# Kernel tuning notes

Measured on AMD Instinct MI355X. Metric: run time of the kernel, lower is better.

Reference implementation:

```python
import jax, jax.numpy as jnp
import numpy as np

NQ = 8
DIM = 2 ** NQ  # 256 amplitudes
HALF_PI = float(np.pi / 2)

CNOT_M = jnp.array([[1, 0, 0, 0], [0, 1, 0, 0], [0, 0, 0, 1], [0, 0, 1, 0]], dtype=jnp.complex64)
SWAP_M = jnp.array([[1, 0, 0, 0], [0, 0, 1, 0], [0, 1, 0, 0], [0, 0, 0, 1]], dtype=jnp.complex64)

# PauliZ sign vectors per wire; wire 0 is the most-significant bit (PennyLane convention)
_bits = (np.arange(DIM)[None, :] >> (NQ - 1 - np.arange(NQ))[:, None]) & 1
ZSIGNS = jnp.asarray(1.0 - 2.0 * _bits, dtype=jnp.float32)  # [NQ, DIM]


def _rx(t):
    c = jnp.cos(0.5 * t).astype(jnp.complex64)
    s = (-1j * jnp.sin(0.5 * t)).astype(jnp.complex64)
    return jnp.stack([jnp.stack([c, s]), jnp.stack([s, c])])


def _ry(t):
    c = jnp.cos(0.5 * t).astype(jnp.complex64)
    s = jnp.sin(0.5 * t).astype(jnp.complex64)
    return jnp.stack([jnp.stack([c, -s]), jnp.stack([s, c])])


def _rz(t):
    e0 = jnp.exp(-0.5j * t).astype(jnp.complex64)
    e1 = jnp.exp(0.5j * t).astype(jnp.complex64)
    z = jnp.zeros((), jnp.complex64)
    return jnp.stack([jnp.stack([e0, z]), jnp.stack([z, e1])])


def _ixx(t):
    c = jnp.cos(0.5 * t).astype(jnp.complex64)
    s = (-1j * jnp.sin(0.5 * t)).astype(jnp.complex64)
    z = jnp.zeros((), jnp.complex64)
    return jnp.stack([jnp.stack([c, z, z, s]), jnp.stack([z, c, s, z]),
                      jnp.stack([z, s, c, z]), jnp.stack([s, z, z, c])])


def _apply_1q(psi, U, w):
    # psi: [B] + [2]*NQ ; apply 2x2 U on wire w
    psi = jnp.moveaxis(psi, 1 + w, -1)
    psi = psi @ U.T
    return jnp.moveaxis(psi, -1, 1 + w)


def _apply_2q(psi, U, w1, w2):
    # apply 4x4 U on wires (w1, w2); w1 is the more-significant wire of U
    psi = jnp.moveaxis(psi, (1 + w1, 1 + w2), (-2, -1))
    shp = psi.shape
    psi = (psi.reshape(shp[:-2] + (4,)) @ U.T).reshape(shp)
    return jnp.moveaxis(psi, (-2, -1), (1 + w1, 1 + w2))


def _edges_from_coupling(coupling):
    # Mirrors the torch code: threshold min-max normalized coupling at 0.5.
    # This is a non-differentiable, data-dependent circuit-structure decision,
    # so it is resolved on concrete values (as the Python ifs do in torch).
    c = np.asarray(jax.device_get(coupling), dtype=np.float64)
    cn = (c - c.min()) / (c.max() - c.min())
    adj = cn > 0.5
    return [(i, j) for i in range(NQ) for j in range(i + 1, NQ) if adj[i, j]]


def _conv(psi, i, j, p):
    psi = _apply_1q(psi, _rz(jnp.float32(-HALF_PI)), j)
    psi = _apply_2q(psi, CNOT_M, j, i)  # CNOT control=j target=i
    psi = _apply_1q(psi, _rz(p[0]), i)
    psi = _apply_1q(psi, _ry(p[1]), j)
    psi = _apply_2q(psi, CNOT_M, i, j)
    psi = _apply_1q(psi, _ry(p[2]), j)
    psi = _apply_2q(psi, CNOT_M, j, i)
    psi = _apply_1q(psi, _rz(jnp.float32(HALF_PI)), i)
    return psi


def _pool(psi, i, j, p):
    psi = _apply_1q(psi, _rz(jnp.float32(-HALF_PI)), j)
    psi = _apply_2q(psi, CNOT_M, j, i)
    psi = _apply_1q(psi, _rz(p[0]), i)
    psi = _apply_1q(psi, _ry(p[1]), j)
    psi = _apply_2q(psi, CNOT_M, i, j)
    psi = _apply_1q(psi, _ry(p[2]), j)
    return psi


def _circuit(x, weights, coupling, edges):
    B = x.shape[0]
    # AmplitudeEmbedding(normalize=True)
    psi = (x / jnp.linalg.norm(x, axis=1, keepdims=True)).astype(jnp.complex64)
    psi = psi.reshape((B,) + (2,) * NQ)
    for i in range(NQ):
        psi = _apply_1q(psi, _rx(weights[i]), i)
        psi = _apply_1q(psi, _ry(weights[i + NQ]), i)
        psi = _apply_1q(psi, _rz(weights[i + 2 * NQ]), i)
    for i in range(NQ):
        for j in range(i + 1, NQ):
            psi = _apply_2q(psi, _ixx(coupling[i, j]), i, j)
    widx = 3 * NQ
    for (i, j) in edges:
        nonadjacent = abs(i - j) != 1
        if nonadjacent:
            psi = _apply_2q(psi, SWAP_M, i, j)
        psi = _conv(psi, i, j, weights[widx:widx + 3])
        psi = _pool(psi, i, j, weights[widx + 3:widx + 6])
        widx += 6
        if nonadjacent:
            psi = _apply_2q(psi, SWAP_M, i, j)
    psi_f = psi.reshape(B, DIM)
    probs = psi_f.real ** 2 + psi_f.imag ** 2  # [B, DIM]
    return probs @ ZSIGNS.T  # [B, NQ] expval(PauliZ(i))


def setup_inputs() -> dict:
    B = 65536
    key = jax.random.key(0)
    k1, k2, k3 = jax.random.split(key, 3)
    x = jax.random.normal(k1, (B, DIM), dtype=jnp.float32)
    weights = jax.random.normal(k2, (3 * NQ + 6 * 28,), dtype=jnp.float32)  # 192: max edges = C(8,2)=28
    coupling = jax.random.normal(k3, (NQ, NQ), dtype=jnp.float32)
    return {"x": x, "weights": weights, "coupling": coupling}


def reference(x, weights, coupling):
    edges = _edges_from_coupling(coupling)
    return _circuit(x, weights, coupling, edges)
```

## Files before the change

kernel.cpp:

```cpp
#include <hip/hip_runtime.h>

#define HP 1.57079632679489662f

typedef float f32x4 __attribute__((ext_vector_type(4)));
typedef short sh4 __attribute__((ext_vector_type(4)));

__device__ __forceinline__ unsigned short f2bf(float f) {
  unsigned int u = __builtin_bit_cast(unsigned int, f);
  u += 0x7fffu + ((u >> 16) & 1u);
  return (unsigned short)(u >> 16);
}

__device__ __forceinline__ void rowswap4(float (&mr)[4][4], float (&mi)[4][4], int a, int b) {
#pragma unroll
  for (int c = 0; c < 4; c++) {
    float tr = mr[a][c]; mr[a][c] = mr[b][c]; mr[b][c] = tr;
    float ti = mi[a][c]; mi[a][c] = mi[b][c]; mi[b][c] = ti;
  }
}

__device__ __forceinline__ void absorb_rz(float (&mr)[4][4], float (&mi)[4][4], float t, int bitpos) {
  float ch = cosf(0.5f * t), sh = sinf(0.5f * t);
#pragma unroll
  for (int r = 0; r < 4; r++) {
    float ph = ((r >> bitpos) & 1) ? sh : -sh;
#pragma unroll
    for (int c = 0; c < 4; c++) {
      float ar = mr[r][c], ai = mi[r][c];
      mr[r][c] = ch * ar - ph * ai;
      mi[r][c] = ch * ai + ph * ar;
    }
  }
}

__device__ __forceinline__ void absorb_ry(float (&mr)[4][4], float (&mi)[4][4], float t, int bitpos) {
  float ch = cosf(0.5f * t), sh = sinf(0.5f * t);
#pragma unroll
  for (int r = 0; r < 4; r++) {
    if ((r >> bitpos) & 1) continue;
    int rb = r | (1 << bitpos);
#pragma unroll
    for (int c = 0; c < 4; c++) {
      float ar = mr[r][c], ai = mi[r][c];
      float br = mr[rb][c], bi = mi[rb][c];
      mr[r][c]  = ch * ar - sh * br;  mi[r][c]  = ch * ai - sh * bi;
      mr[rb][c] = sh * ar + ch * br;  mi[rb][c] = sh * ai + ch * bi;
    }
  }
}


__global__ __launch_bounds__(64) void prep_kernel(const float* __restrict__ wt,
                                                  const float* __restrict__ coup,
                                                  void* __restrict__ wsv) {
  const int lane = threadIdx.x;
  int* meta  = (int*)wsv;
  float* Q1  = (float*)((char*)wsv + 256);
  float* E4  = (float*)((char*)wsv + 512);

  double mn = 1e300, mx = -1e300;
  for (int k = 0; k < 64; k++) {
    double v = (double)coup[k];
    mn = v < mn ? v : mn;
    mx = v > mx ? v : mx;
  }
  int cnt = 0, myi = -1, myj = -1;
  for (int i = 0; i < 8; i++)
    for (int j = i + 1; j < 8; j++) {
      double cn = ((double)coup[i * 8 + j] - mn) / (mx - mn);
      if (cn > 0.5) {
        if (cnt == lane) { myi = i; myj = j; }
        cnt++;
      }
    }
  if (lane == 0) meta[0] = cnt;

  if (lane < 8) {
    float tx = wt[lane], ty = wt[8 + lane], tz = wt[16 + lane];
    float cx = cosf(0.5f * tx), sx = sinf(0.5f * tx);
    float cy = cosf(0.5f * ty), sy = sinf(0.5f * ty);
    float cz = cosf(0.5f * tz), sz = sinf(0.5f * tz);
    float m00r = cy * cx,  m00i = sy * sx;
    float m01r = -sy * cx, m01i = -cy * sx;
    float m10r = sy * cx,  m10i = -cy * sx;
    float m11r = cy * cx,  m11i = -sy * sx;
    float* q = Q1 + lane * 8;
    q[0] = cz * m00r + sz * m00i; q[1] = cz * m00i - sz * m00r;
    q[2] = cz * m01r + sz * m01i; q[3] = cz * m01i - sz * m01r;
    q[4] = cz * m10r - sz * m10i; q[5] = cz * m10i + sz * m10r;
    q[6] = cz * m11r - sz * m11i; q[7] = cz * m11i + sz * m11r;
  }

  if (lane < cnt && lane < 28) {
    float mr[4][4], mi[4][4];
#pragma unroll
    for (int r = 0; r < 4; r++)
#pragma unroll
      for (int c = 0; c < 4; c++) { mr[r][c] = (r == c) ? 1.f : 0.f; mi[r][c] = 0.f; }

    bool nonadj = (myj - myi) != 1;
    int wb = 24 + 6 * lane;

    if (nonadj) rowswap4(mr, mi, 1, 2);
    absorb_rz(mr, mi, -HP, 0);
    rowswap4(mr, mi, 1, 3);
    absorb_rz(mr, mi, wt[wb + 0], 1);
    absorb_ry(mr, mi, wt[wb + 1], 0);
    rowswap4(mr, mi, 2, 3);
    absorb_ry(mr, mi, wt[wb + 2], 0);
    rowswap4(mr, mi, 1, 3);
    absorb_rz(mr, mi, HP, 1);
    absorb_rz(mr, mi, -HP, 0);
    rowswap4(mr, mi, 1, 3);
    absorb_rz(mr, mi, wt[wb + 3], 1);
    absorb_ry(mr, mi, wt[wb + 4], 0);
    rowswap4(mr, mi, 2, 3);
    absorb_ry(mr, mi, wt[wb + 5], 0);
    if (nonadj) rowswap4(mr, mi, 1, 2);

    float* e = E4 + lane * 32;
#pragma unroll
    for (int r = 0; r < 4; r++)
#pragma unroll
      for (int c = 0; c < 4; c++) {
        e[(r * 4 + c) * 2]     = mr[r][c];
        e[(r * 4 + c) * 2 + 1] = mi[r][c];
      }
    meta[1 + 2 * lane] = myi;
    meta[2 + 2 * lane] = myj;
  }
}

__global__ __launch_bounds__(256) void build_u_kernel(const float* __restrict__ coup,
                                                      void* __restrict__ wsv) {
  const int* meta = (const int*)wsv;
  const float* Q1 = (const float*)((char*)wsv + 256);
  const float* E4 = (const float*)((char*)wsv + 512);
  unsigned char* Ub = (unsigned char*)wsv + 4096;

  const int c = blockIdx.x;
  const int tid = threadIdx.x;

  __shared__ float2 s[256];
  s[tid] = make_float2(tid == c ? 1.f : 0.f, 0.f);
  __syncthreads();

  for (int wi = 0; wi < 8; wi++) {
    const float* M = Q1 + wi * 8;
    int p = 7 - wi;
    float2 a0 = s[tid & ~(1 << p)];
    float2 a1 = s[tid | (1 << p)];
    int b = (tid >> p) & 1;
    float m0r = M[(b * 2 + 0) * 2], m0i = M[(b * 2 + 0) * 2 + 1];
    float m1r = M[(b * 2 + 1) * 2], m1i = M[(b * 2 + 1) * 2 + 1];
    float nr = m0r * a0.x - m0i * a0.y + m1r * a1.x - m1i * a1.y;
    float ni = m0r * a0.y + m0i * a0.x + m1r * a1.y + m1i * a1.x;
    __syncthreads();
    s[tid] = make_float2(nr, ni);
    __syncthreads();
  }

  for (int i = 0; i < 8; i++)
    for (int j = i + 1; j < 8; j++) {
      float t = coup[i * 8 + j];
      float ch = cosf(0.5f * t), sn = sinf(0.5f * t);
      int mask = (1 << (7 - i)) | (1 << (7 - j));
      float2 a = s[tid];
      float2 b = s[tid ^ mask];
      __syncthreads();
      s[tid] = make_float2(ch * a.x + sn * b.y, ch * a.y - sn * b.x);
      __syncthreads();
    }

  int ne = meta[0];
  for (int e = 0; e < ne; e++) {
    int i = meta[1 + 2 * e], j = meta[2 + 2 * e];
    int p1 = 7 - i, p2 = 7 - j;
    int m1 = 1 << p1, m2 = 1 << p2;
    int b = ((tid >> p1) & 1) * 2 + ((tid >> p2) & 1);
    int base = tid & ~(m1 | m2);
    float2 a0 = s[base];
    float2 a1 = s[base | m2];
    float2 a2 = s[base | m1];
    float2 a3 = s[base | m1 | m2];
    const float* M = E4 + e * 32 + b * 8;
    float nr = M[0] * a0.x - M[1] * a0.y + M[2] * a1.x - M[3] * a1.y
             + M[4] * a2.x - M[5] * a2.y + M[6] * a3.x - M[7] * a3.y;
    float ni = M[0] * a0.y + M[1] * a0.x + M[2] * a1.y + M[3] * a1.x
             + M[4] * a2.y + M[5] * a2.x + M[6] * a3.y + M[7] * a3.x;
    __syncthreads();
    s[tid] = make_float2(nr, ni);
    __syncthreads();
  }

  {
    int ks = c >> 5, kc = c & 31;
    int sb = (kc >> 4) & 1, lg2 = (kc >> 2) & 3, ii = kc & 3;
    int p = (lg2 + tid) & 3;
    unsigned char* base = Ub + (size_t)ks * 32768 + (size_t)(2 * tid) * 64 + p * 16 + sb * 8 + ii * 2;
    *(unsigned short*)(base)      = f2bf(s[tid].x);
    *(unsigned short*)(base + 64) = f2bf(s[tid].y);
  }
}

#define MFMA_STEP(KS, AREG)                                                              \
  {                                                                                      \
    uint4 bq[4];                                                                         \
    _Pragma("unroll")                                                                    \
    for (int nf = 0; nf < 4; nf++) {                                                     \
      const int n = nf * 16 + lm;                                                        \
      int byte = (n * 512 + (KS) * 64 + lg * 16) ^ ((n & 7) << 4);                       \
      bq[nf] = *reinterpret_cast<const uint4*>(&smem[byte]);                             \
    }                                                                                    \
    _Pragma("unroll")                                                                    \
    for (int mf = 0; mf < 4; mf++) {                                                     \
      const sh4 alo = __builtin_bit_cast(sh4, make_uint2(AREG[mf].x, AREG[mf].y));       \
      const sh4 ahi = __builtin_bit_cast(sh4, make_uint2(AREG[mf].z, AREG[mf].w));       \
      _Pragma("unroll")                                                                  \
      for (int nf = 0; nf < 4; nf++) {                                                   \
        const sh4 blo = __builtin_bit_cast(sh4, make_uint2(bq[nf].x, bq[nf].y));         \
        const sh4 bhi = __builtin_bit_cast(sh4, make_uint2(bq[nf].z, bq[nf].w));         \
        acc[mf][nf] = __builtin_amdgcn_mfma_f32_16x16x16bf16_1k(alo, blo, acc[mf][nf], 0, 0, 0); \
        acc[mf][nf] = __builtin_amdgcn_mfma_f32_16x16x16bf16_1k(ahi, bhi, acc[mf][nf], 0, 0, 0); \
      }                                                                                  \
    }                                                                                    \
  }

__global__ __launch_bounds__(512, 4) void gemm_l2(const float* __restrict__ x,
                                                  const void* __restrict__ wsv,
                                                  float* __restrict__ out) {
  const unsigned char* Ub = (const unsigned char*)wsv + 4096;
  __shared__ __align__(16) unsigned char smem[32768];

  const int tid = threadIdx.x;
  const int tile = blockIdx.x;
  const int wv = tid >> 6;
  const int lane = tid & 63;
  const int lm = lane & 15;
  const int lg = lane >> 4;

  {
    const int rl = tid >> 3;
    const int seg = tid & 7;
    const float4* xs = (const float4*)(x + (size_t)(tile * 64 + rl) * 256 + seg * 32);
    float4 v[8];
    float ss = 0.f;
#pragma unroll
    for (int i = 0; i < 8; i++) {
      v[i] = xs[i];
      ss += v[i].x * v[i].x + v[i].y * v[i].y + v[i].z * v[i].z + v[i].w * v[i].w;
    }
    ss += __shfl_xor(ss, 1);
    ss += __shfl_xor(ss, 2);
    ss += __shfl_xor(ss, 4);
    float inv = 1.0f / sqrtf(ss);
    const float* vf = (const float*)v;
#pragma unroll
    for (int u = 0; u < 4; u++) {
      unsigned short h[8];
#pragma unroll
      for (int j = 0; j < 8; j++)
        h[j] = f2bf(vf[16 * (j >> 2) + 4 * u + (j & 3)] * inv);
      uint4 pack;
      pack.x = (unsigned)h[0] | ((unsigned)h[1] << 16);
      pack.y = (unsigned)h[2] | ((unsigned)h[3] << 16);
      pack.z = (unsigned)h[4] | ((unsigned)h[5] << 16);
      pack.w = (unsigned)h[6] | ((unsigned)h[7] << 16);
      int byte = (rl * 512 + seg * 64 + u * 16) ^ ((rl & 7) << 4);
      *reinterpret_cast<uint4*>(&smem[byte]) = pack;
    }
  }

  const unsigned char* abase[4];
#pragma unroll
  for (int mf = 0; mf < 4; mf++) {
    const int m = wv * 64 + mf * 16 + lm;
    const int p = (lg + (m >> 1)) & 3;
    abase[mf] = Ub + (size_t)m * 64 + p * 16;
  }

  f32x4 acc[4][4] = {};
  uint4 aP[4], aQ[4];
#pragma unroll
  for (int mf = 0; mf < 4; mf++) aP[mf] = *reinterpret_cast<const uint4*>(abase[mf]);

  __syncthreads();

#pragma unroll
  for (int kk = 0; kk < 4; kk++) {
#pragma unroll
    for (int mf = 0; mf < 4; mf++)
      aQ[mf] = *reinterpret_cast<const uint4*>(abase[mf] + (size_t)(2 * kk + 1) * 32768);
    MFMA_STEP(2 * kk, aP);
    if (kk < 3) {
#pragma unroll
      for (int mf = 0; mf < 4; mf++)
        aP[mf] = *reinterpret_cast<const uint4*>(abase[mf] + (size_t)(2 * kk + 2) * 32768);
    }
    MFMA_STEP(2 * kk + 1, aQ);
  }
  __syncthreads();

  float pq[4][8];
#pragma unroll
  for (int nf = 0; nf < 4; nf++) {
    float T = 0.f, S7 = 0.f, S4 = 0.f, S3 = 0.f;
#pragma unroll
    for (int mf = 0; mf < 4; mf++) {
      f32x4 a = acc[mf][nf];
      float p0 = a[0] * a[0] + a[1] * a[1];
      float p1 = a[2] * a[2] + a[3] * a[3];
      float sp = p0 + p1, d = p0 - p1;
      T += sp;
      S7 += d;
      S4 += (mf & 1) ? -sp : sp;
      S3 += (mf & 2) ? -sp : sp;
    }
    pq[nf][7] = S7;
    pq[nf][6] = (lg & 1) ? -T : T;
    pq[nf][5] = (lg & 2) ? -T : T;
    pq[nf][4] = S4;
    pq[nf][3] = S3;
    pq[nf][2] = (wv & 1) ? -T : T;
    pq[nf][1] = (wv & 2) ? -T : T;
    pq[nf][0] = (wv & 4) ? -T : T;
  }
#pragma unroll
  for (int nf = 0; nf < 4; nf++)
#pragma unroll
    for (int k = 0; k < 8; k++) {
      pq[nf][k] += __shfl_xor(pq[nf][k], 16);
      pq[nf][k] += __shfl_xor(pq[nf][k], 32);
    }

  float* part = (float*)smem;
  if (lg == 0) {
#pragma unroll
    for (int nf = 0; nf < 4; nf++) {
      float* dst = part + (wv * 64 + nf * 16 + lm) * 8;
#pragma unroll
      for (int k = 0; k < 8; k++) dst[k] = pq[nf][k];
    }
  }
  __syncthreads();
  {
    int b = tid >> 3, q = tid & 7;
    float v2 = 0.f;
#pragma unroll
    for (int w2 = 0; w2 < 8; w2++) v2 += part[(w2 * 64 + b) * 8 + q];
    out[(size_t)(tile * 64 + b) * 8 + q] = v2;
  }
}

extern "C" void kernel_launch(void* const* d_in, const int* in_sizes, int n_in,
                              void* d_out, int out_size, void* d_ws, size_t ws_size,
                              hipStream_t stream) {
  const float* x    = (const float*)d_in[0];
  const float* wt   = (const float*)d_in[1];
  const float* coup = (const float*)d_in[2];
  float* out = (float*)d_out;

  prep_kernel<<<1, 64, 0, stream>>>(wt, coup, d_ws);
  build_u_kernel<<<256, 256, 0, stream>>>(coup, d_ws);
  gemm_l2<<<1024, 512, 0, stream>>>(x, d_ws, out);
}
```

Baseline: 64.44 us.

## Fold prep into build_u kernel, hoist A loads, add setprio and native bf16 conversion

```diff
diff --git a/kernel.cpp b/kernel.cpp
--- a/kernel.cpp
+++ b/kernel.cpp
@@ -4,6 +4,7 @@
 
 typedef float f32x4 __attribute__((ext_vector_type(4)));
 typedef short sh4 __attribute__((ext_vector_type(4)));
+typedef __bf16 bf16x8 __attribute__((ext_vector_type(8)));
 
 __device__ __forceinline__ unsigned short f2bf(float f) {
   unsigned int u = __builtin_bit_cast(unsigned int, f);
@@ -50,103 +51,97 @@
 }
 
 
-__global__ __launch_bounds__(64) void prep_kernel(const float* __restrict__ wt,
-                                                  const float* __restrict__ coup,
-                                                  void* __restrict__ wsv) {
-  const int lane = threadIdx.x;
-  int* meta  = (int*)wsv;
-  float* Q1  = (float*)((char*)wsv + 256);
-  float* E4  = (float*)((char*)wsv + 512);
-
-  double mn = 1e300, mx = -1e300;
-  for (int k = 0; k < 64; k++) {
-    double v = (double)coup[k];
-    mn = v < mn ? v : mn;
-    mx = v > mx ? v : mx;
-  }
-  int cnt = 0, myi = -1, myj = -1;
-  for (int i = 0; i < 8; i++)
-    for (int j = i + 1; j < 8; j++) {
-      double cn = ((double)coup[i * 8 + j] - mn) / (mx - mn);
-      if (cn > 0.5) {
-        if (cnt == lane) { myi = i; myj = j; }
-        cnt++;
-      }
-    }
-  if (lane == 0) meta[0] = cnt;
-
-  if (lane < 8) {
-    float tx = wt[lane], ty = wt[8 + lane], tz = wt[16 + lane];
-    float cx = cosf(0.5f * tx), sx = sinf(0.5f * tx);
-    float cy = cosf(0.5f * ty), sy = sinf(0.5f * ty);
-    float cz = cosf(0.5f * tz), sz = sinf(0.5f * tz);
-    float m00r = cy * cx,  m00i = sy * sx;
-    float m01r = -sy * cx, m01i = -cy * sx;
-    float m10r = sy * cx,  m10i = -cy * sx;
-    float m11r = cy * cx,  m11i = -sy * sx;
-    float* q = Q1 + lane * 8;
-    q[0] = cz * m00r + sz * m00i; q[1] = cz * m00i - sz * m00r;
-    q[2] = cz * m01r + sz * m01i; q[3] = cz * m01i - sz * m01r;
-    q[4] = cz * m10r - sz * m10i; q[5] = cz * m10i + sz * m10r;
-    q[6] = cz * m11r - sz * m11i; q[7] = cz * m11i + sz * m11r;
-  }
-
-  if (lane < cnt && lane < 28) {
-    float mr[4][4], mi[4][4];
-#pragma unroll
-    for (int r = 0; r < 4; r++)
-#pragma unroll
-      for (int c = 0; c < 4; c++) { mr[r][c] = (r == c) ? 1.f : 0.f; mi[r][c] = 0.f; }
-
-    bool nonadj = (myj - myi) != 1;
-    int wb = 24 + 6 * lane;
-
-    if (nonadj) rowswap4(mr, mi, 1, 2);
-    absorb_rz(mr, mi, -HP, 0);
-    rowswap4(mr, mi, 1, 3);
-    absorb_rz(mr, mi, wt[wb + 0], 1);
-    absorb_ry(mr, mi, wt[wb + 1], 0);
-    rowswap4(mr, mi, 2, 3);
-    absorb_ry(mr, mi, wt[wb + 2], 0);
-    rowswap4(mr, mi, 1, 3);
-    absorb_rz(mr, mi, HP, 1);
-    absorb_rz(mr, mi, -HP, 0);
-    rowswap4(mr, mi, 1, 3);
-    absorb_rz(mr, mi, wt[wb + 3], 1);
-    absorb_ry(mr, mi, wt[wb + 4], 0);
-    rowswap4(mr, mi, 2, 3);
-    absorb_ry(mr, mi, wt[wb + 5], 0);
-    if (nonadj) rowswap4(mr, mi, 1, 2);
-
-    float* e = E4 + lane * 32;
-#pragma unroll
-    for (int r = 0; r < 4; r++)
-#pragma unroll
-      for (int c = 0; c < 4; c++) {
-        e[(r * 4 + c) * 2]     = mr[r][c];
-        e[(r * 4 + c) * 2 + 1] = mi[r][c];
-      }
-    meta[1 + 2 * lane] = myi;
-    meta[2 + 2 * lane] = myj;
-  }
-}
-
-__global__ __launch_bounds__(256) void build_u_kernel(const float* __restrict__ coup,
+__global__ __launch_bounds__(256) void build_u_kernel(const float* __restrict__ wt,
+                                                      const float* __restrict__ coup,
                                                       void* __restrict__ wsv) {
-  const int* meta = (const int*)wsv;
-  const float* Q1 = (const float*)((char*)wsv + 256);
-  const float* E4 = (const float*)((char*)wsv + 512);
   unsigned char* Ub = (unsigned char*)wsv + 4096;
-
   const int c = blockIdx.x;
   const int tid = threadIdx.x;
 
   __shared__ float2 s[256];
+  __shared__ float Q1s[64];
+  __shared__ float E4s[28 * 32];
+  __shared__ int metas[57];
+
+  {
+    double mn = 1e300, mx = -1e300;
+    for (int k = 0; k < 64; k++) {
+      double v = (double)coup[k];
+      mn = v < mn ? v : mn;
+      mx = v > mx ? v : mx;
+    }
+    int cnt = 0, myi = -1, myj = -1;
+    for (int i = 0; i < 8; i++)
+      for (int j = i + 1; j < 8; j++) {
+        double cn = ((double)coup[i * 8 + j] - mn) / (mx - mn);
+        if (cn > 0.5) {
+          if (cnt == tid) { myi = i; myj = j; }
+          cnt++;
+        }
+      }
+    if (tid == 0) metas[0] = cnt;
+
+    if (tid < 8) {
+      float tx = wt[tid], ty = wt[8 + tid], tz = wt[16 + tid];
+      float cx = cosf(0.5f * tx), sx = sinf(0.5f * tx);
+      float cy = cosf(0.5f * ty), sy = sinf(0.5f * ty);
+      float cz = cosf(0.5f * tz), sz = sinf(0.5f * tz);
+      float m00r = cy * cx,  m00i = sy * sx;
+      float m01r = -sy * cx, m01i = -cy * sx;
+      float m10r = sy * cx,  m10i = -cy * sx;
+      float m11r = cy * cx,  m11i = -sy * sx;
+      float* q = Q1s + tid * 8;
+      q[0] = cz * m00r + sz * m00i; q[1] = cz * m00i - sz * m00r;
+      q[2] = cz * m01r + sz * m01i; q[3] = cz * m01i - sz * m01r;
+      q[4] = cz * m10r - sz * m10i; q[5] = cz * m10i + sz * m10r;
+      q[6] = cz * m11r - sz * m11i; q[7] = cz * m11i + sz * m11r;
+    }
+
+    if (tid < cnt && tid < 28) {
+      float mr[4][4], mi[4][4];
+#pragma unroll
+      for (int r = 0; r < 4; r++)
+#pragma unroll
+        for (int cc = 0; cc < 4; cc++) { mr[r][cc] = (r == cc) ? 1.f : 0.f; mi[r][cc] = 0.f; }
+
+      bool nonadj = (myj - myi) != 1;
+      int wb = 24 + 6 * tid;
+
+      if (nonadj) rowswap4(mr, mi, 1, 2);
+      absorb_rz(mr, mi, -HP, 0);
+      rowswap4(mr, mi, 1, 3);
+      absorb_rz(mr, mi, wt[wb + 0], 1);
+      absorb_ry(mr, mi, wt[wb + 1], 0);
+      rowswap4(mr, mi, 2, 3);
+      absorb_ry(mr, mi, wt[wb + 2], 0);
+      rowswap4(mr, mi, 1, 3);
+      absorb_rz(mr, mi, HP, 1);
+      absorb_rz(mr, mi, -HP, 0);
+      rowswap4(mr, mi, 1, 3);
+      absorb_rz(mr, mi, wt[wb + 3], 1);
+      absorb_ry(mr, mi, wt[wb + 4], 0);
+      rowswap4(mr, mi, 2, 3);
+      absorb_ry(mr, mi, wt[wb + 5], 0);
+      if (nonadj) rowswap4(mr, mi, 1, 2);
+
+      float* e = E4s + tid * 32;
+#pragma unroll
+      for (int r = 0; r < 4; r++)
+#pragma unroll
+        for (int cc = 0; cc < 4; cc++) {
+          e[(r * 4 + cc) * 2]     = mr[r][cc];
+          e[(r * 4 + cc) * 2 + 1] = mi[r][cc];
+        }
+      metas[1 + 2 * tid] = myi;
+      metas[2 + 2 * tid] = myj;
+    }
+  }
+
   s[tid] = make_float2(tid == c ? 1.f : 0.f, 0.f);
   __syncthreads();
 
   for (int wi = 0; wi < 8; wi++) {
-    const float* M = Q1 + wi * 8;
+    const float* M = Q1s + wi * 8;
     int p = 7 - wi;
     float2 a0 = s[tid & ~(1 << p)];
     float2 a1 = s[tid | (1 << p)];
@@ -172,9 +167,9 @@
       __syncthreads();
     }
 
-  int ne = meta[0];
+  int ne = metas[0];
   for (int e = 0; e < ne; e++) {
-    int i = meta[1 + 2 * e], j = meta[2 + 2 * e];
+    int i = metas[1 + 2 * e], j = metas[2 + 2 * e];
     int p1 = 7 - i, p2 = 7 - j;
     int m1 = 1 << p1, m2 = 1 << p2;
     int b = ((tid >> p1) & 1) * 2 + ((tid >> p2) & 1);
@@ -183,7 +178,7 @@
     float2 a1 = s[base | m2];
     float2 a2 = s[base | m1];
     float2 a3 = s[base | m1 | m2];
-    const float* M = E4 + e * 32 + b * 8;
+    const float* M = E4s + e * 32 + b * 8;
     float nr = M[0] * a0.x - M[1] * a0.y + M[2] * a1.x - M[3] * a1.y
              + M[4] * a2.x - M[5] * a2.y + M[6] * a3.x - M[7] * a3.y;
     float ni = M[0] * a0.y + M[1] * a0.x + M[2] * a1.y + M[3] * a1.x
@@ -212,6 +207,7 @@
       int byte = (n * 512 + (KS) * 64 + lg * 16) ^ ((n & 7) << 4);                       \
       bq[nf] = *reinterpret_cast<const uint4*>(&smem[byte]);                             \
     }                                                                                    \
+    __builtin_amdgcn_s_setprio(1);                                                       \
     _Pragma("unroll")                                                                    \
     for (int mf = 0; mf < 4; mf++) {                                                     \
       const sh4 alo = __builtin_bit_cast(sh4, make_uint2(AREG[mf].x, AREG[mf].y));       \
@@ -224,6 +220,7 @@
         acc[mf][nf] = __builtin_amdgcn_mfma_f32_16x16x16bf16_1k(ahi, bhi, acc[mf][nf], 0, 0, 0); \
       }                                                                                  \
     }                                                                                    \
+    __builtin_amdgcn_s_setprio(0);                                                       \
   }
 
 __global__ __launch_bounds__(512, 4) void gemm_l2(const float* __restrict__ x,
@@ -239,6 +236,17 @@
   const int lm = lane & 15;
   const int lg = lane >> 4;
 
+  const unsigned char* abase[4];
+#pragma unroll
+  for (int mf = 0; mf < 4; mf++) {
+    const int m = wv * 64 + mf * 16 + lm;
+    const int p = (lg + (m >> 1)) & 3;
+    abase[mf] = Ub + (size_t)m * 64 + p * 16;
+  }
+  uint4 aP[4], aQ[4];
+#pragma unroll
+  for (int mf = 0; mf < 4; mf++) aP[mf] = *reinterpret_cast<const uint4*>(abase[mf]);
+
   {
     const int rl = tid >> 3;
     const int seg = tid & 7;
@@ -257,33 +265,17 @@
     const float* vf = (const float*)v;
 #pragma unroll
     for (int u = 0; u < 4; u++) {
-      unsigned short h[8];
+      bf16x8 w;
 #pragma unroll
       for (int j = 0; j < 8; j++)
-        h[j] = f2bf(vf[16 * (j >> 2) + 4 * u + (j & 3)] * inv);
-      uint4 pack;
-      pack.x = (unsigned)h[0] | ((unsigned)h[1] << 16);
-      pack.y = (unsigned)h[2] | ((unsigned)h[3] << 16);
-      pack.z = (unsigned)h[4] | ((unsigned)h[5] << 16);
-      pack.w = (unsigned)h[6] | ((unsigned)h[7] << 16);
+        w[j] = (__bf16)(vf[16 * (j >> 2) + 4 * u + (j & 3)] * inv);
+      uint4 pack = __builtin_bit_cast(uint4, w);
       int byte = (rl * 512 + seg * 64 + u * 16) ^ ((rl & 7) << 4);
       *reinterpret_cast<uint4*>(&smem[byte]) = pack;
     }
   }
 
-  const unsigned char* abase[4];
-#pragma unroll
-  for (int mf = 0; mf < 4; mf++) {
-    const int m = wv * 64 + mf * 16 + lm;
-    const int p = (lg + (m >> 1)) & 3;
-    abase[mf] = Ub + (size_t)m * 64 + p * 16;
-  }
-
   f32x4 acc[4][4] = {};
-  uint4 aP[4], aQ[4];
-#pragma unroll
-  for (int mf = 0; mf < 4; mf++) aP[mf] = *reinterpret_cast<const uint4*>(abase[mf]);
-
   __syncthreads();
 
 #pragma unroll
@@ -360,7 +352,6 @@
   const float* coup = (const float*)d_in[2];
   float* out = (float*)d_out;
 
-  prep_kernel<<<1, 64, 0, stream>>>(wt, coup, d_ws);
-  build_u_kernel<<<256, 256, 0, stream>>>(coup, d_ws);
+  build_u_kernel<<<256, 256, 0, stream>>>(wt, coup, d_ws);
   gemm_l2<<<1024, 512, 0, stream>>>(x, d_ws, out);
 }
```

Measured after the change: 58.57 us. 1.1x faster.
